# Optimization experiments

Hardware: AMD Instinct MI355X
Metric: run time of the kernel (lower is better)

The kernel has to match this reference:

```python
import jax, jax.numpy as jnp
import numpy as np

D_MODEL, N_HEADS, D_K, D_V, D_FF, SEQ = 2048, 16, 128, 128, 8192, 2048
EPS = 1e-5


def _layernorm(x, g, b):
    mu = jnp.mean(x, axis=-1, keepdims=True)
    var = jnp.var(x, axis=-1, keepdims=True)
    return (x - mu) * jax.lax.rsqrt(var + EPS) * g + b


def setup_inputs() -> dict:
    key = jax.random.key(0)
    ks = jax.random.split(key, 10)
    return {
        "x": jax.random.normal(ks[0], (SEQ, D_MODEL), jnp.float32),
        # per-head projections stacked over heads (matches num_heads separate DotProductAttention params)
        "wq": jax.random.normal(ks[1], (N_HEADS, D_MODEL, D_K), jnp.float32),
        "wk": jax.random.normal(ks[2], (N_HEADS, D_MODEL, D_K), jnp.float32),
        "wv": jax.random.normal(ks[3], (N_HEADS, D_MODEL, D_V), jnp.float32),
        "w_proj": jax.random.normal(ks[4], (N_HEADS * D_V, D_MODEL), jnp.float32),
        "g1": jnp.ones((D_MODEL,), jnp.float32),
        "b1": jnp.zeros((D_MODEL,), jnp.float32),
        "fc1_w": jax.random.normal(ks[5], (D_MODEL, D_FF), jnp.float32) * 0.02,
        "fc1_b": jnp.zeros((D_FF,), jnp.float32),
        "fc2_w": jax.random.normal(ks[6], (D_FF, D_MODEL), jnp.float32) * 0.02,
        "fc2_b": jnp.zeros((D_MODEL,), jnp.float32),
        "g2": jnp.ones((D_MODEL,), jnp.float32),
        "b2": jnp.zeros((D_MODEL,), jnp.float32),
    }


def reference(x, wq, wk, wv, w_proj, g1, b1, fc1_w, fc1_b, fc2_w, fc2_b, g2, b2):
    # multi-head attention (heads batched via einsum; same math as the per-head loop)
    q = jnp.einsum("sd,hdk->hsk", x, wq)
    k = jnp.einsum("sd,hdk->hsk", x, wk)
    v = jnp.einsum("sd,hdv->hsv", x, wv)
    scores = jnp.einsum("hsk,htk->hst", q, k) * (1.0 / np.sqrt(D_K))
    attn = jax.nn.softmax(scores, axis=-1)
    heads = jnp.einsum("hst,htv->hsv", attn, v)  # [H,S,Dv]
    concat = jnp.transpose(heads, (1, 0, 2)).reshape(SEQ, N_HEADS * D_V)
    attn_out = concat @ w_proj
    # residual + LayerNorm (dropout=0 -> identity)
    h = _layernorm(x + attn_out, g1, b1)
    # FFN with ReLU
    ff = jax.nn.relu(h @ fc1_w + fc1_b) @ fc2_w + fc2_b
    return _layernorm(h + ff, g2, b2)
```

## Files before the change

### kernel.cpp

```cpp
#include <hip/hip_runtime.h>


typedef __bf16 bf16;
typedef __attribute__((ext_vector_type(8))) __bf16 bf16x8;
typedef __attribute__((ext_vector_type(4))) __bf16 bf16x4;
typedef __attribute__((ext_vector_type(4))) float f32x4;

#define MFMA(a, b, c) __builtin_amdgcn_mfma_f32_16x16x32_bf16((a), (b), (c), 0, 0, 0)
#define NEG_INF (-3.402823466e38f)

__device__ __forceinline__ void cp16(void* lds, const void* g) {
  __builtin_amdgcn_global_load_lds(
      (const __attribute__((address_space(1))) unsigned int*)g,
      (__attribute__((address_space(3))) unsigned int*)lds, 16, 0, 0);
}

#define SBAR() __builtin_amdgcn_sched_barrier(0)
#define GBAR()                              \
  do {                                      \
    asm volatile("" ::: "memory");          \
    __builtin_amdgcn_s_barrier();           \
    asm volatile("" ::: "memory");          \
  } while (0)
#define LGKM0()                                         \
  do {                                                  \
    asm volatile("s_waitcnt lgkmcnt(0)" ::: "memory");  \
    __builtin_amdgcn_sched_barrier(0);                  \
  } while (0)
#define VMC6()                                          \
  do {                                                  \
    asm volatile("s_waitcnt vmcnt(6)" ::: "memory");    \
    __builtin_amdgcn_sched_barrier(0);                  \
  } while (0)


__global__ void k_split_x(const float* __restrict__ x, bf16* __restrict__ xh,
                          bf16* __restrict__ xl) {
  int i = blockIdx.x * 256 + threadIdx.x;
  f32x4 v = ((const f32x4*)x)[i];
  bf16x4 h, l;
#pragma unroll
  for (int j = 0; j < 4; ++j) {
    bf16 hi = (bf16)v[j];
    h[j] = hi;
    l[j] = (bf16)(v[j] - (float)hi);
  }
  ((bf16x4*)xh)[i] = h;
  ((bf16x4*)xl)[i] = l;
}

template <bool SPLIT>
__global__ void k_tcvt(const float* __restrict__ in, bf16* __restrict__ oh,
                       bf16* __restrict__ ol, int R, int C) {
  __shared__ float t[64][65];
  long zoff = (long)blockIdx.z * R * C;
  int c0 = blockIdx.x * 64, r0 = blockIdx.y * 64;
  int cc = threadIdx.x & 63, rr = threadIdx.x >> 6;
#pragma unroll
  for (int i = 0; i < 16; ++i) {
    int r = i * 4 + rr;
    t[r][cc] = in[zoff + (long)(r0 + r) * C + c0 + cc];
  }
  __syncthreads();
#pragma unroll
  for (int i = 0; i < 16; ++i) {
    int orow = i * 4 + rr;
    float v = t[cc][orow];
    long oidx = zoff + (long)(c0 + orow) * R + r0 + cc;
    bf16 hi = (bf16)v;
    oh[oidx] = hi;
    if (SPLIT) ol[oidx] = (bf16)(v - (float)hi);
  }
}

__global__ void k_combine4(const float* __restrict__ p, long pstr,
                           bf16* __restrict__ o) {
  int i = blockIdx.x * 256 + threadIdx.x;
  f32x4 v = ((const f32x4*)p)[i];
#pragma unroll
  for (int zz = 1; zz < 4; ++zz) v += ((const f32x4*)(p + zz * pstr))[i];
  bf16x4 ob;
#pragma unroll
  for (int j = 0; j < 4; ++j) ob[j] = (bf16)v[j];
  ((bf16x4*)o)[i] = ob;
}

template <int EPI>
__global__ __launch_bounds__(512, 1) void k_gemm8(
    const bf16* __restrict__ A, const bf16* __restrict__ B,
    float* __restrict__ Cf, bf16* __restrict__ Cb,
    const float* __restrict__ bias, int M, int N, int K, int nsplit) {
  __shared__ char lds[131072];
  const int tid = threadIdx.x, w = tid >> 6, l = tid & 63;
  const int l16 = l & 15, lg = l >> 4;
  const int wr = w >> 2, wc = w & 3;
  const long bm0 = (long)blockIdx.y * 256, bn0 = (long)blockIdx.x * 256;
  const int z = blockIdx.z;
  const int ksz = K / nsplit, kbeg = z * ksz;
  const int nt = ksz >> 6;
  const long lK = K;

  const int srow = w * 8 + (l >> 3);
  const int sslot = (l & 7) ^ (l >> 3);

  auto STAGE = [&](int bufp, int isB, int h, int tt) {
    int tc = tt < nt ? tt : nt - 1;
    char* dst = lds + bufp * 65536 + isB * 32768 + h * 16384 + w * 1024;
    const bf16* G = isB ? B : A;
    long r0 = (isB ? bn0 : bm0) + h * 128 + srow;
    const bf16* src = G + r0 * lK + kbeg + tc * 64 + sslot * 8;
    cp16(dst, src);
    cp16(dst + 8192, src + 64 * lK);
  };
  auto LDA = [&](int bufp, int mf, int ks) -> bf16x8 {
    int inrow = (mf & 3) * 32 + wr * 16 + l16;
    int byo = bufp * 65536 + (mf >> 2) * 16384 + inrow * 128 +
              ((((ks << 2) + lg) ^ (inrow & 7)) << 4);
    return *(const bf16x8*)(lds + byo);
  };
  auto LDB = [&](int bufp, int nf, int ks) -> bf16x8 {
    int inrow = (nf & 1) * 64 + wc * 16 + l16;
    int byo = bufp * 65536 + 32768 + (nf >> 1) * 16384 + inrow * 128 +
              ((((ks << 2) + lg) ^ (inrow & 7)) << 4);
    return *(const bf16x8*)(lds + byo);
  };

  f32x4 acc[8][4];
#pragma unroll
  for (int mf = 0; mf < 8; ++mf)
#pragma unroll
    for (int nf = 0; nf < 4; ++nf)
#pragma unroll
      for (int j = 0; j < 4; ++j) acc[mf][nf][j] = 0.f;

  STAGE(0, 0, 0, 0);
  STAGE(0, 1, 0, 0);
  STAGE(0, 0, 1, 0);
  STAGE(0, 1, 1, 0);
  STAGE(1, 1, 0, 1);
  STAGE(1, 0, 1, 1);
  STAGE(1, 1, 1, 1);
  SBAR();
  VMC6();
  GBAR();

  bf16x8 a[4][2], b[2][2];
  for (int t = 0; t < nt; ++t) {
    const int cb = t & 1, nb = cb ^ 1;
#pragma unroll
    for (int mf = 0; mf < 4; ++mf)
#pragma unroll
      for (int ks = 0; ks < 2; ++ks) a[mf][ks] = LDA(cb, mf, ks);
#pragma unroll
    for (int nf = 0; nf < 2; ++nf)
#pragma unroll
      for (int ks = 0; ks < 2; ++ks) b[nf][ks] = LDB(cb, nf, ks);
    STAGE(nb, 0, 0, t + 1);
    SBAR();
    GBAR();
    LGKM0();
    __builtin_amdgcn_s_setprio(1);
#pragma unroll
    for (int mf = 0; mf < 4; ++mf)
#pragma unroll
      for (int nf = 0; nf < 2; ++nf)
#pragma unroll
        for (int ks = 0; ks < 2; ++ks)
          acc[mf][nf] = MFMA(a[mf][ks], b[nf][ks], acc[mf][nf]);
    __builtin_amdgcn_s_setprio(0);
    GBAR();
#pragma unroll
    for (int mf = 0; mf < 4; ++mf)
#pragma unroll
      for (int ks = 0; ks < 2; ++ks) a[mf][ks] = LDA(cb, mf + 4, ks);
    STAGE(cb, 1, 0, t + 2);
    SBAR();
    GBAR();
    LGKM0();
    __builtin_amdgcn_s_setprio(1);
#pragma unroll
    for (int mf = 0; mf < 4; ++mf)
#pragma unroll
      for (int nf = 0; nf < 2; ++nf)
#pragma unroll
        for (int ks = 0; ks < 2; ++ks)
          acc[mf + 4][nf] = MFMA(a[mf][ks], b[nf][ks], acc[mf + 4][nf]);
    __builtin_amdgcn_s_setprio(0);
    GBAR();
#pragma unroll
    for (int nf = 0; nf < 2; ++nf)
#pragma unroll
      for (int ks = 0; ks < 2; ++ks) b[nf][ks] = LDB(cb, nf + 2, ks);
    GBAR();
    LGKM0();
    __builtin_amdgcn_s_setprio(1);
#pragma unroll
    for (int mf = 0; mf < 4; ++mf)
#pragma unroll
      for (int nf = 0; nf < 2; ++nf)
#pragma unroll
        for (int ks = 0; ks < 2; ++ks)
          acc[mf + 4][nf + 2] = MFMA(a[mf][ks], b[nf][ks], acc[mf + 4][nf + 2]);
    __builtin_amdgcn_s_setprio(0);
    GBAR();
#pragma unroll
    for (int mf = 0; mf < 4; ++mf)
#pragma unroll
      for (int ks = 0; ks < 2; ++ks) a[mf][ks] = LDA(cb, mf, ks);
    STAGE(cb, 0, 1, t + 2);
    STAGE(cb, 1, 1, t + 2);
    SBAR();
    VMC6();
    GBAR();
    LGKM0();
    __builtin_amdgcn_s_setprio(1);
#pragma unroll
    for (int mf = 0; mf < 4; ++mf)
#pragma unroll
      for (int nf = 0; nf < 2; ++nf)
#pragma unroll
        for (int ks = 0; ks < 2; ++ks)
          acc[mf][nf + 2] = MFMA(a[mf][ks], b[nf][ks], acc[mf][nf + 2]);
    __builtin_amdgcn_s_setprio(0);
    GBAR();
  }
  asm volatile("s_waitcnt vmcnt(0) lgkmcnt(0)" ::: "memory");

#pragma unroll
  for (int mf = 0; mf < 8; ++mf)
#pragma unroll
    for (int nf = 0; nf < 4; ++nf) {
      long col = bn0 + nf * 64 + wc * 16 + l16;
      float bv = (EPI == 2) ? bias[col] : 0.f;
#pragma unroll
      for (int jj = 0; jj < 4; ++jj) {
        long row = bm0 + mf * 32 + wr * 16 + lg * 4 + jj;
        float v = acc[mf][nf][jj];
        if (EPI == 0) {
          Cf[(long)z * M * N + row * N + col] = v;
        } else {
          v = fmaxf(v + bv, 0.f);
          Cb[row * N + col] = (bf16)v;
        }
      }
    }
}

__global__ __launch_bounds__(256, 2) void k_gemm_split3(
    const bf16* __restrict__ Ah, const bf16* __restrict__ Al,
    const bf16* __restrict__ Bh, const bf16* __restrict__ Bl,
    bf16* __restrict__ Ch, bf16* __restrict__ Cl,
    int M, int N, int K, float scale, int scale_ncols) {
  __shared__ bf16 sAh[4096], sAl[4096], sBh[4096], sBl[4096];
  const int tid = threadIdx.x, w = tid >> 6, l = tid & 63;
  const int l16 = l & 15, lg = l >> 4;
  const int wr = w >> 1, wc = w & 1;
  const long bm0 = (long)blockIdx.y * 128, bn0 = (long)blockIdx.x * 128;
  f32x4 acc[4][4];
#pragma unroll
  for (int m = 0; m < 4; ++m)
#pragma unroll
    for (int n = 0; n < 4; ++n)
#pragma unroll
      for (int j = 0; j < 4; ++j) acc[m][n][j] = 0.f;

  for (int kt = 0; kt < K; kt += 32) {
    __syncthreads();
#pragma unroll
    for (int i = 0; i < 2; ++i) {
      int c = (w * 2 + i) * 64 + l;
      int row = c >> 2, seg = c & 3;
      long ao = (bm0 + row) * K + kt + seg * 8;
      long bo = (bn0 + row) * K + kt + seg * 8;
      int db = (w * 2 + i) * 512;
      cp16(&sAh[db], &Ah[ao]);
      cp16(&sAl[db], &Al[ao]);
      cp16(&sBh[db], &Bh[bo]);
      cp16(&sBl[db], &Bl[bo]);
    }
    __syncthreads();
    bf16x8 ah[4], al[4], bh[4], bl[4];
#pragma unroll
    for (int m = 0; m < 4; ++m) {
      int off = (wr * 64 + m * 16 + l16) * 32 + lg * 8;
      ah[m] = *(const bf16x8*)&sAh[off];
      al[m] = *(const bf16x8*)&sAl[off];
    }
#pragma unroll
    for (int n = 0; n < 4; ++n) {
      int off = (wc * 64 + n * 16 + l16) * 32 + lg * 8;
      bh[n] = *(const bf16x8*)&sBh[off];
      bl[n] = *(const bf16x8*)&sBl[off];
    }
#pragma unroll
    for (int m = 0; m < 4; ++m)
#pragma unroll
      for (int n = 0; n < 4; ++n) {
        acc[m][n] = MFMA(ah[m], bh[n], acc[m][n]);
        acc[m][n] = MFMA(ah[m], bl[n], acc[m][n]);
        acc[m][n] = MFMA(al[m], bh[n], acc[m][n]);
      }
  }
#pragma unroll
  for (int m = 0; m < 4; ++m)
#pragma unroll
    for (int n = 0; n < 4; ++n) {
      long col = bn0 + wc * 64 + n * 16 + l16;
      float sc = (col < scale_ncols) ? scale : 1.0f;
#pragma unroll
      for (int j = 0; j < 4; ++j) {
        long row = bm0 + wr * 64 + m * 16 + lg * 4 + j;
        float v = acc[m][n][j] * sc;
        bf16 hi = (bf16)v;
        Ch[row * N + col] = hi;
        Cl[row * N + col] = (bf16)(v - (float)hi);
      }
    }
}

__global__ __launch_bounds__(256, 2) void k_flash(
    const bf16* __restrict__ Qh, const bf16* __restrict__ Ql,
    const bf16* __restrict__ Kh, const bf16* __restrict__ Kl,
    const bf16* __restrict__ Vt, bf16* __restrict__ Oc) {
  __shared__ bf16 sm[28672];
  bf16* sKh = sm;
  bf16* sKl = sm + 8192;
  bf16* sVt = sm + 16384;
  bf16* sP = sm + 24576;
  const int tid = threadIdx.x, w = tid >> 6, l = tid & 63;
  const int l16 = l & 15, lg = l >> 4;
  const int head = blockIdx.y;
  const long q0 = (long)blockIdx.x * 64;

  bf16x8 qh_r[4], ql_r[4];
#pragma unroll
  for (int kk = 0; kk < 4; ++kk) {
    long off = (q0 + w * 16 + l16) * 4096 + head * 128 + kk * 32 + lg * 8;
    qh_r[kk] = *(const bf16x8*)&Qh[off];
    ql_r[kk] = *(const bf16x8*)&Ql[off];
  }

  f32x4 acc_o[8];
#pragma unroll
  for (int n = 0; n < 8; ++n)
#pragma unroll
    for (int j = 0; j < 4; ++j) acc_o[n][j] = 0.f;
  float mrow[4], lrow[4];
#pragma unroll
  for (int j = 0; j < 4; ++j) {
    mrow[j] = NEG_INF;
    lrow[j] = 0.f;
  }

  for (int t0 = 0; t0 < 2048; t0 += 64) {
    __syncthreads();
#pragma unroll
    for (int i = 0; i < 4; ++i) {
      int c = (w * 4 + i) * 64 + l;
      int rk = c >> 4, sk = (c & 15) ^ (rk & 7);
      long ko = (long)(t0 + rk) * 4096 + head * 128 + sk * 8;
      int db = (w * 4 + i) * 512;
      cp16(&sKh[db], &Kh[ko]);
      cp16(&sKl[db], &Kl[ko]);
      int rv = c >> 3, sv = (c & 7) ^ (rv & 7);
      long vo = (long)(head * 128 + rv) * 2048 + t0 + sv * 8;
      cp16(&sVt[db], &Vt[vo]);
    }
    __syncthreads();

    f32x4 s[4];
#pragma unroll
    for (int n = 0; n < 4; ++n)
#pragma unroll
      for (int j = 0; j < 4; ++j) s[n][j] = 0.f;
#pragma unroll
    for (int kk = 0; kk < 4; ++kk) {
      bf16x8 bh[4], bl[4];
#pragma unroll
      for (int n = 0; n < 4; ++n) {
        int r = n * 16 + l16;
        int byo = r * 256 + (((kk * 4 + lg) ^ (r & 7)) << 4);
        bh[n] = *(const bf16x8*)((const char*)sKh + byo);
        bl[n] = *(const bf16x8*)((const char*)sKl + byo);
      }
#pragma unroll
      for (int n = 0; n < 4; ++n) {
        s[n] = MFMA(qh_r[kk], bh[n], s[n]);
        s[n] = MFMA(qh_r[kk], bl[n], s[n]);
        s[n] = MFMA(ql_r[kk], bh[n], s[n]);
      }
    }

#pragma unroll
    for (int j = 0; j < 4; ++j) {
      float mx = fmaxf(fmaxf(s[0][j], s[1][j]), fmaxf(s[2][j], s[3][j]));
      mx = fmaxf(mx, __shfl_xor(mx, 1));
      mx = fmaxf(mx, __shfl_xor(mx, 2));
      mx = fmaxf(mx, __shfl_xor(mx, 4));
      mx = fmaxf(mx, __shfl_xor(mx, 8));
      float mo = mrow[j];
      float mn = fmaxf(mo, mx);
      mrow[j] = mn;
      float f = __expf(mo - mn);
      int prow = w * 16 + lg * 4 + j;
      float ssum = 0.f;
#pragma unroll
      for (int n = 0; n < 4; ++n) {
        float p = __expf(s[n][j] - mn);
        ssum += p;
        int byo = prow * 128 + (((n * 16 + l16) * 2) ^ ((prow & 7) << 4));
        *(bf16*)((char*)sP + byo) = (bf16)p;
      }
      ssum += __shfl_xor(ssum, 1);
      ssum += __shfl_xor(ssum, 2);
      ssum += __shfl_xor(ssum, 4);
      ssum += __shfl_xor(ssum, 8);
      lrow[j] = lrow[j] * f + ssum;
#pragma unroll
      for (int n = 0; n < 8; ++n) acc_o[n][j] *= f;
    }

#pragma unroll
    for (int kk = 0; kk < 2; ++kk) {
      bf16x8 pa, bv[8];
      {
        int r = w * 16 + l16;
        int byo = r * 128 + (((kk * 4 + lg) ^ (r & 7)) << 4);
        pa = *(const bf16x8*)((const char*)sP + byo);
      }
#pragma unroll
      for (int n = 0; n < 8; ++n) {
        int r = n * 16 + l16;
        int byo = r * 128 + (((kk * 4 + lg) ^ (r & 7)) << 4);
        bv[n] = *(const bf16x8*)((const char*)sVt + byo);
      }
#pragma unroll
      for (int n = 0; n < 8; ++n) acc_o[n] = MFMA(pa, bv[n], acc_o[n]);
    }
  }

#pragma unroll
  for (int j = 0; j < 4; ++j) {
    float rinv = 1.f / lrow[j];
    long row = q0 + w * 16 + lg * 4 + j;
#pragma unroll
    for (int n = 0; n < 8; ++n)
      Oc[row * 2048 + head * 128 + n * 16 + l16] = (bf16)(acc_o[n][j] * rinv);
  }
}

__global__ __launch_bounds__(256) void k_add_ln(
    const float* __restrict__ a, const float* __restrict__ p, long pstr,
    int np, const float* __restrict__ bias, const float* __restrict__ g,
    const float* __restrict__ be, float* __restrict__ o32,
    bf16* __restrict__ obf) {
  __shared__ float red[8];
  int row = blockIdx.x, tid = threadIdx.x;
  const float* pa = a + (long)row * 2048;
  f32x4 v[2];
  float sum = 0.f, sq = 0.f;
#pragma unroll
  for (int i = 0; i < 2; ++i) {
    int idx = i * 1024 + tid * 4;
    v[i] = *(const f32x4*)(pa + idx);
    for (int zz = 0; zz < np; ++zz)
      v[i] += *(const f32x4*)(p + zz * pstr + (long)row * 2048 + idx);
    if (bias != nullptr) v[i] += *(const f32x4*)(bias + idx);
#pragma unroll
    for (int j = 0; j < 4; ++j) {
      sum += v[i][j];
      sq += v[i][j] * v[i][j];
    }
  }
#pragma unroll
  for (int o = 1; o < 64; o <<= 1) {
    sum += __shfl_xor(sum, o);
    sq += __shfl_xor(sq, o);
  }
  int w = tid >> 6;
  if ((tid & 63) == 0) {
    red[w * 2] = sum;
    red[w * 2 + 1] = sq;
  }
  __syncthreads();
  sum = red[0] + red[2] + red[4] + red[6];
  sq = red[1] + red[3] + red[5] + red[7];
  float mu = sum * (1.f / 2048.f);
  float var = sq * (1.f / 2048.f) - mu * mu;
  float rs = rsqrtf(var + 1e-5f);
#pragma unroll
  for (int i = 0; i < 2; ++i) {
    int idx = i * 1024 + tid * 4;
    f32x4 vg = *(const f32x4*)(g + idx);
    f32x4 vb = *(const f32x4*)(be + idx);
    f32x4 o;
#pragma unroll
    for (int j = 0; j < 4; ++j) o[j] = (v[i][j] - mu) * rs * vg[j] + vb[j];
    *(f32x4*)(o32 + (long)row * 2048 + idx) = o;
    if (obf != nullptr) {
      bf16x4 ob;
#pragma unroll
      for (int j = 0; j < 4; ++j) ob[j] = (bf16)o[j];
      *(bf16x4*)(obf + (long)row * 2048 + idx) = ob;
    }
  }
}

extern "C" void kernel_launch(void* const* d_in, const int* in_sizes, int n_in,
                              void* d_out, int out_size, void* d_ws, size_t ws_size,
                              hipStream_t stream) {
  const float* x    = (const float*)d_in[0];
  const float* wq   = (const float*)d_in[1];
  const float* wk   = (const float*)d_in[2];
  const float* wv   = (const float*)d_in[3];
  const float* wp   = (const float*)d_in[4];
  const float* g1   = (const float*)d_in[5];
  const float* b1   = (const float*)d_in[6];
  const float* fc1w = (const float*)d_in[7];
  const float* fc1b = (const float*)d_in[8];
  const float* fc2w = (const float*)d_in[9];
  const float* fc2b = (const float*)d_in[10];
  const float* g2   = (const float*)d_in[11];
  const float* b2   = (const float*)d_in[12];
  float* out = (float*)d_out;

  char* ws = (char*)d_ws;
  const size_t MB = 1024 * 1024;
  if (ws_size < 216 * MB) return;
  const long W4M = 4L * 1024 * 1024;

  bf16* xh    = (bf16*)(ws + 0 * MB);
  bf16* xl    = (bf16*)(ws + 8 * MB);
  bf16* qk_bh = (bf16*)(ws + 16 * MB);
  bf16* qk_bl = (bf16*)(ws + 32 * MB);
  bf16* wvt   = (bf16*)(ws + 48 * MB);
  bf16* wpt   = (bf16*)(ws + 56 * MB);
  bf16* fc1t  = (bf16*)(ws + 64 * MB);
  bf16* fc2t  = (bf16*)(ws + 96 * MB);
  float* vtp  = (float*)(ws + 128 * MB);
  bf16* vtb   = (bf16*)(ws + 192 * MB);
  bf16* qkh   = (bf16*)(ws + 128 * MB);
  bf16* qkl   = (bf16*)(ws + 144 * MB);
  bf16* cc    = (bf16*)(ws + 200 * MB);
  float* aop  = (float*)(ws + 128 * MB);
  float* h32  = (float*)(ws + 160 * MB);
  bf16*  hbf  = (bf16*)(ws + 208 * MB);
  bf16*  ff1  = (bf16*)(ws + 128 * MB);
  float* ffp  = (float*)(ws + 0 * MB);
  h32 = (float*)(ws + 192 * MB);
  const long PSTR = 4194304L;

  k_split_x<<<4096, 256, 0, stream>>>(x, xh, xl);
  k_tcvt<true ><<<dim3(2, 32, 16), 256, 0, stream>>>(wq, qk_bh, qk_bl, 2048, 128);
  k_tcvt<true ><<<dim3(2, 32, 16), 256, 0, stream>>>(wk, qk_bh + W4M, qk_bl + W4M,
                                                     2048, 128);
  k_tcvt<false><<<dim3(2, 32, 16), 256, 0, stream>>>(wv, wvt, nullptr, 2048, 128);
  k_tcvt<false><<<dim3(32, 32, 1), 256, 0, stream>>>(wp, wpt, nullptr, 2048, 2048);
  k_tcvt<false><<<dim3(128, 32, 1), 256, 0, stream>>>(fc1w, fc1t, nullptr, 2048, 8192);
  k_tcvt<false><<<dim3(32, 128, 1), 256, 0, stream>>>(fc2w, fc2t, nullptr, 8192, 2048);

  k_gemm8<0><<<dim3(8, 8, 4), 512, 0, stream>>>(
      wvt, xh, vtp, nullptr, nullptr, 2048, 2048, 2048, 4);
  k_combine4<<<4096, 256, 0, stream>>>(vtp, PSTR, vtb);
  k_gemm_split3<<<dim3(32, 16), 256, 0, stream>>>(
      xh, xl, qk_bh, qk_bl, qkh, qkl, 2048, 4096, 2048,
      0.08838834764831845f, 2048);
  k_flash<<<dim3(32, 16), 256, 0, stream>>>(qkh, qkl, qkh + 2048, qkl + 2048,
                                            vtb, cc);
  k_gemm8<0><<<dim3(8, 8, 4), 512, 0, stream>>>(
      cc, wpt, aop, nullptr, nullptr, 2048, 2048, 2048, 4);
  k_add_ln<<<2048, 256, 0, stream>>>(x, aop, PSTR, 4, nullptr, g1, b1, h32, hbf);
  k_gemm8<2><<<dim3(32, 8, 1), 512, 0, stream>>>(
      hbf, fc1t, nullptr, ff1, fc1b, 2048, 8192, 2048, 1);
  k_gemm8<0><<<dim3(8, 8, 4), 512, 0, stream>>>(
      ff1, fc2t, ffp, nullptr, nullptr, 2048, 2048, 8192, 4);
  k_add_ln<<<2048, 256, 0, stream>>>(h32, ffp, PSTR, 4, fc2b, g2, b2, out, nullptr);
}
```

Baseline: 529.4 us.

## Pipeline split-precision QK GEMM and register-prefetch K/V tiles in flash attention

Replaces the simple split-bf16 QK projection GEMM with an 8-wave, 128x256-tile kernel. It double-buffers global-to-LDS loads with swizzled layout and interleaves MFMA phases with the next tile's staging, using barriers and priority hints. The flash attention kernel now prefetches the next K/V tile into registers while computing the current one, then writes it to LDS, overlapping global latency with compute. This costs more LDS, more registers and more barriers, which may reduce occupancy.

```diff
diff --git a/kernel.cpp b/kernel.cpp
--- a/kernel.cpp
+++ b/kernel.cpp
@@ -5,6 +5,7 @@
 typedef __attribute__((ext_vector_type(8))) __bf16 bf16x8;
 typedef __attribute__((ext_vector_type(4))) __bf16 bf16x4;
 typedef __attribute__((ext_vector_type(4))) float f32x4;
+typedef __attribute__((ext_vector_type(4))) unsigned int u32x4;
 
 #define MFMA(a, b, c) __builtin_amdgcn_mfma_f32_16x16x32_bf16((a), (b), (c), 0, 0, 0)
 #define NEG_INF (-3.402823466e38f)
@@ -246,71 +247,163 @@
     }
 }
 
-__global__ __launch_bounds__(256, 2) void k_gemm_split3(
-    const bf16* __restrict__ Ah, const bf16* __restrict__ Al,
-    const bf16* __restrict__ Bh, const bf16* __restrict__ Bl,
+__global__ __launch_bounds__(512, 1) void k_split8(
+    const bf16* __restrict__ Ah_g, const bf16* __restrict__ Al_g,
+    const bf16* __restrict__ Bh_g, const bf16* __restrict__ Bl_g,
     bf16* __restrict__ Ch, bf16* __restrict__ Cl,
     int M, int N, int K, float scale, int scale_ncols) {
-  __shared__ bf16 sAh[4096], sAl[4096], sBh[4096], sBl[4096];
+  __shared__ char lds[98304];
   const int tid = threadIdx.x, w = tid >> 6, l = tid & 63;
   const int l16 = l & 15, lg = l >> 4;
-  const int wr = w >> 1, wc = w & 1;
-  const long bm0 = (long)blockIdx.y * 128, bn0 = (long)blockIdx.x * 128;
+  const int wr = w >> 2, wc = w & 3;
+  const long bm0 = (long)blockIdx.y * 128, bn0 = (long)blockIdx.x * 256;
+  const int nt = K >> 5;
+  const long lK = K;
+
+  const int srcrow = tid >> 2;
+  const int ss = (tid & 3) ^ ((tid >> 3) & 3);
+
+  auto STG_A = [&](int bufp, int isLo, int tt) {
+    int tc = tt < nt ? tt : nt - 1;
+    char* dst = lds + bufp * 49152 + isLo * 8192 + tid * 16;
+    const bf16* G = isLo ? Al_g : Ah_g;
+    cp16(dst, &G[(bm0 + srcrow) * lK + tc * 32 + ss * 8]);
+  };
+  auto STG_B = [&](int bufp, int isLo, int half, int tt) {
+    int tc = tt < nt ? tt : nt - 1;
+    char* dst = lds + bufp * 49152 + 16384 + isLo * 16384 + half * 8192 + tid * 16;
+    const bf16* G = isLo ? Bl_g : Bh_g;
+    cp16(dst, &G[(bn0 + half * 128 + srcrow) * lK + tc * 32 + ss * 8]);
+  };
+  auto LDA8 = [&](int bufp, int mf, int isLo) -> bf16x8 {
+    int row = mf * 32 + wr * 16 + l16;
+    int byo = bufp * 49152 + isLo * 8192 + row * 64 +
+              ((lg ^ ((row >> 1) & 3)) << 4);
+    return *(const bf16x8*)(lds + byo);
+  };
+  auto LDB8 = [&](int bufp, int nf, int isLo) -> bf16x8 {
+    int row = nf * 64 + wc * 16 + l16;
+    int byo = bufp * 49152 + 16384 + isLo * 16384 + row * 64 +
+              ((lg ^ ((row >> 1) & 3)) << 4);
+    return *(const bf16x8*)(lds + byo);
+  };
+
   f32x4 acc[4][4];
 #pragma unroll
-  for (int m = 0; m < 4; ++m)
-#pragma unroll
-    for (int n = 0; n < 4; ++n)
-#pragma unroll
-      for (int j = 0; j < 4; ++j) acc[m][n][j] = 0.f;
-
-  for (int kt = 0; kt < K; kt += 32) {
-    __syncthreads();
-#pragma unroll
-    for (int i = 0; i < 2; ++i) {
-      int c = (w * 2 + i) * 64 + l;
-      int row = c >> 2, seg = c & 3;
-      long ao = (bm0 + row) * K + kt + seg * 8;
-      long bo = (bn0 + row) * K + kt + seg * 8;
-      int db = (w * 2 + i) * 512;
-      cp16(&sAh[db], &Ah[ao]);
-      cp16(&sAl[db], &Al[ao]);
-      cp16(&sBh[db], &Bh[bo]);
-      cp16(&sBl[db], &Bl[bo]);
-    }
-    __syncthreads();
-    bf16x8 ah[4], al[4], bh[4], bl[4];
-#pragma unroll
-    for (int m = 0; m < 4; ++m) {
-      int off = (wr * 64 + m * 16 + l16) * 32 + lg * 8;
-      ah[m] = *(const bf16x8*)&sAh[off];
-      al[m] = *(const bf16x8*)&sAl[off];
-    }
-#pragma unroll
-    for (int n = 0; n < 4; ++n) {
-      int off = (wc * 64 + n * 16 + l16) * 32 + lg * 8;
-      bh[n] = *(const bf16x8*)&sBh[off];
-      bl[n] = *(const bf16x8*)&sBl[off];
-    }
-#pragma unroll
-    for (int m = 0; m < 4; ++m)
-#pragma unroll
-      for (int n = 0; n < 4; ++n) {
-        acc[m][n] = MFMA(ah[m], bh[n], acc[m][n]);
-        acc[m][n] = MFMA(ah[m], bl[n], acc[m][n]);
-        acc[m][n] = MFMA(al[m], bh[n], acc[m][n]);
-      }
-  }
-#pragma unroll
-  for (int m = 0; m < 4; ++m)
-#pragma unroll
-    for (int n = 0; n < 4; ++n) {
-      long col = bn0 + wc * 64 + n * 16 + l16;
+  for (int mf = 0; mf < 4; ++mf)
+#pragma unroll
+    for (int nf = 0; nf < 4; ++nf)
+#pragma unroll
+      for (int j = 0; j < 4; ++j) acc[mf][nf][j] = 0.f;
+
+  STG_B(0, 0, 0, 0); STG_B(0, 1, 0, 0);
+  STG_A(0, 0, 0);    STG_A(0, 1, 0);
+  STG_B(0, 0, 1, 0); STG_B(0, 1, 1, 0);
+  STG_B(1, 0, 0, 1); STG_B(1, 1, 0, 1);
+  STG_A(1, 0, 1);    STG_A(1, 1, 1);
+  STG_B(1, 0, 1, 1); STG_B(1, 1, 1, 1);
+  SBAR();
+  VMC6();
+  GBAR();
+
+  bf16x8 ah[4], al[4], bh[2], bl[2];
+  for (int t = 0; t < nt; ++t) {
+    const int cb = t & 1;
+#pragma unroll
+    for (int mf = 0; mf < 2; ++mf) {
+      ah[mf] = LDA8(cb, mf, 0);
+      al[mf] = LDA8(cb, mf, 1);
+    }
+#pragma unroll
+    for (int nf = 0; nf < 2; ++nf) {
+      bh[nf] = LDB8(cb, nf, 0);
+      bl[nf] = LDB8(cb, nf, 1);
+    }
+    SBAR();
+    GBAR();
+    LGKM0();
+    __builtin_amdgcn_s_setprio(1);
+#pragma unroll
+    for (int mf = 0; mf < 2; ++mf)
+#pragma unroll
+      for (int nf = 0; nf < 2; ++nf) {
+        acc[mf][nf] = MFMA(ah[mf], bh[nf], acc[mf][nf]);
+        acc[mf][nf] = MFMA(ah[mf], bl[nf], acc[mf][nf]);
+        acc[mf][nf] = MFMA(al[mf], bh[nf], acc[mf][nf]);
+      }
+    __builtin_amdgcn_s_setprio(0);
+    GBAR();
+#pragma unroll
+    for (int mf = 2; mf < 4; ++mf) {
+      ah[mf] = LDA8(cb, mf, 0);
+      al[mf] = LDA8(cb, mf, 1);
+    }
+    STG_B(cb, 0, 0, t + 2);
+    STG_B(cb, 1, 0, t + 2);
+    SBAR();
+    GBAR();
+    LGKM0();
+    __builtin_amdgcn_s_setprio(1);
+#pragma unroll
+    for (int mf = 2; mf < 4; ++mf)
+#pragma unroll
+      for (int nf = 0; nf < 2; ++nf) {
+        acc[mf][nf] = MFMA(ah[mf], bh[nf], acc[mf][nf]);
+        acc[mf][nf] = MFMA(ah[mf], bl[nf], acc[mf][nf]);
+        acc[mf][nf] = MFMA(al[mf], bh[nf], acc[mf][nf]);
+      }
+    __builtin_amdgcn_s_setprio(0);
+    GBAR();
+#pragma unroll
+    for (int nf = 0; nf < 2; ++nf) {
+      bh[nf] = LDB8(cb, nf + 2, 0);
+      bl[nf] = LDB8(cb, nf + 2, 1);
+    }
+    STG_A(cb, 0, t + 2);
+    STG_A(cb, 1, t + 2);
+    SBAR();
+    GBAR();
+    LGKM0();
+    __builtin_amdgcn_s_setprio(1);
+#pragma unroll
+    for (int mf = 2; mf < 4; ++mf)
+#pragma unroll
+      for (int nf = 0; nf < 2; ++nf) {
+        acc[mf][nf + 2] = MFMA(ah[mf], bh[nf], acc[mf][nf + 2]);
+        acc[mf][nf + 2] = MFMA(ah[mf], bl[nf], acc[mf][nf + 2]);
+        acc[mf][nf + 2] = MFMA(al[mf], bh[nf], acc[mf][nf + 2]);
+      }
+    __builtin_amdgcn_s_setprio(0);
+    GBAR();
+    STG_B(cb, 0, 1, t + 2);
+    STG_B(cb, 1, 1, t + 2);
+    SBAR();
+    VMC6();
+    GBAR();
+    __builtin_amdgcn_s_setprio(1);
+#pragma unroll
+    for (int mf = 0; mf < 2; ++mf)
+#pragma unroll
+      for (int nf = 0; nf < 2; ++nf) {
+        acc[mf][nf + 2] = MFMA(ah[mf], bh[nf], acc[mf][nf + 2]);
+        acc[mf][nf + 2] = MFMA(ah[mf], bl[nf], acc[mf][nf + 2]);
+        acc[mf][nf + 2] = MFMA(al[mf], bh[nf], acc[mf][nf + 2]);
+      }
+    __builtin_amdgcn_s_setprio(0);
+    GBAR();
+  }
+  asm volatile("s_waitcnt vmcnt(0) lgkmcnt(0)" ::: "memory");
+
+#pragma unroll
+  for (int mf = 0; mf < 4; ++mf)
+#pragma unroll
+    for (int nf = 0; nf < 4; ++nf) {
+      long col = bn0 + nf * 64 + wc * 16 + l16;
       float sc = (col < scale_ncols) ? scale : 1.0f;
 #pragma unroll
       for (int j = 0; j < 4; ++j) {
-        long row = bm0 + wr * 64 + m * 16 + lg * 4 + j;
-        float v = acc[m][n][j] * sc;
+        long row = bm0 + mf * 32 + wr * 16 + lg * 4 + j;
+        float v = acc[mf][nf][j] * sc;
         bf16 hi = (bf16)v;
         Ch[row * N + col] = hi;
         Cl[row * N + col] = (bf16)(v - (float)hi);
@@ -352,22 +445,29 @@
     lrow[j] = 0.f;
   }
 
-  for (int t0 = 0; t0 < 2048; t0 += 64) {
-    __syncthreads();
+  auto LOADT = [&](u32x4 (&kh)[4], u32x4 (&kl)[4], u32x4 (&vt)[4], int t0) {
 #pragma unroll
     for (int i = 0; i < 4; ++i) {
       int c = (w * 4 + i) * 64 + l;
       int rk = c >> 4, sk = (c & 15) ^ (rk & 7);
       long ko = (long)(t0 + rk) * 4096 + head * 128 + sk * 8;
-      int db = (w * 4 + i) * 512;
-      cp16(&sKh[db], &Kh[ko]);
-      cp16(&sKl[db], &Kl[ko]);
+      kh[i] = *(const u32x4*)&Kh[ko];
+      kl[i] = *(const u32x4*)&Kl[ko];
       int rv = c >> 3, sv = (c & 7) ^ (rv & 7);
       long vo = (long)(head * 128 + rv) * 2048 + t0 + sv * 8;
-      cp16(&sVt[db], &Vt[vo]);
-    }
-    __syncthreads();
-
+      vt[i] = *(const u32x4*)&Vt[vo];
+    }
+  };
+  auto WRITET = [&](u32x4 (&kh)[4], u32x4 (&kl)[4], u32x4 (&vt)[4]) {
+#pragma unroll
+    for (int i = 0; i < 4; ++i) {
+      int db = (w * 4 + i) * 512 + l * 8;
+      *(u32x4*)&sKh[db] = kh[i];
+      *(u32x4*)&sKl[db] = kl[i];
+      *(u32x4*)&sVt[db] = vt[i];
+    }
+  };
+  auto COMPUTE = [&]() {
     f32x4 s[4];
 #pragma unroll
     for (int n = 0; n < 4; ++n)
@@ -390,7 +490,6 @@
         s[n] = MFMA(ql_r[kk], bh[n], s[n]);
       }
     }
-
 #pragma unroll
     for (int j = 0; j < 4; ++j) {
       float mx = fmaxf(fmaxf(s[0][j], s[1][j]), fmaxf(s[2][j], s[3][j]));
@@ -419,7 +518,6 @@
 #pragma unroll
       for (int n = 0; n < 8; ++n) acc_o[n][j] *= f;
     }
-
 #pragma unroll
     for (int kk = 0; kk < 2; ++kk) {
       bf16x8 pa, bv[8];
@@ -437,6 +535,21 @@
 #pragma unroll
       for (int n = 0; n < 8; ++n) acc_o[n] = MFMA(pa, bv[n], acc_o[n]);
     }
+  };
+
+  u32x4 akh[4], akl[4], avt[4], bkh[4], bkl[4], bvt[4];
+  LOADT(akh, akl, avt, 0);
+  for (int tt = 0; tt < 2048; tt += 128) {
+    __syncthreads();
+    WRITET(akh, akl, avt);
+    __syncthreads();
+    LOADT(bkh, bkl, bvt, tt + 64);
+    COMPUTE();
+    __syncthreads();
+    WRITET(bkh, bkl, bvt);
+    __syncthreads();
+    LOADT(akh, akl, avt, (tt + 128 < 2048) ? tt + 128 : 0);
+    COMPUTE();
   }
 
 #pragma unroll
@@ -543,11 +656,10 @@
   bf16* qkl   = (bf16*)(ws + 144 * MB);
   bf16* cc    = (bf16*)(ws + 200 * MB);
   float* aop  = (float*)(ws + 128 * MB);
-  float* h32  = (float*)(ws + 160 * MB);
+  float* h32  = (float*)(ws + 192 * MB);
   bf16*  hbf  = (bf16*)(ws + 208 * MB);
   bf16*  ff1  = (bf16*)(ws + 128 * MB);
   float* ffp  = (float*)(ws + 0 * MB);
-  h32 = (float*)(ws + 192 * MB);
   const long PSTR = 4194304L;
 
   k_split_x<<<4096, 256, 0, stream>>>(x, xh, xl);
@@ -562,7 +674,7 @@
   k_gemm8<0><<<dim3(8, 8, 4), 512, 0, stream>>>(
       wvt, xh, vtp, nullptr, nullptr, 2048, 2048, 2048, 4);
   k_combine4<<<4096, 256, 0, stream>>>(vtp, PSTR, vtb);
-  k_gemm_split3<<<dim3(32, 16), 256, 0, stream>>>(
+  k_split8<<<dim3(16, 16), 512, 0, stream>>>(
       xh, xl, qk_bh, qk_bl, qkh, qkl, 2048, 4096, 2048,
       0.08838834764831845f, 2048);
   k_flash<<<dim3(32, 16), 256, 0, stream>>>(qkh, qkl, qkh + 2048, qkl + 2048,
```

Measured after the change: 543.3 us. +2.6%, slower.
